# Performance work log

Hardware: AMD Instinct MI355X
Metric: run time of the kernel (lower is better)

The kernel has to match this reference:

```python
import jax, jax.numpy as jnp
import numpy as np
from jax import lax

T, B, DIM, N = 1024, 64, 512, 64


def setup_inputs() -> dict:
    key = jax.random.key(0)
    k1, k2 = jax.random.split(key)
    x = jax.random.normal(k1, (T, B, DIM), dtype=jnp.float32)
    # xavier-uniform-like scale for fused projection [4n, dim]
    lim = float(np.sqrt(6.0 / (N + DIM)))
    W_kvqm = jax.random.uniform(k2, (4 * N, DIM), dtype=jnp.float32, minval=-lim, maxval=lim)
    return {
        "x": x,
        "S0": jnp.zeros((B, N, N), dtype=jnp.float32),
        "M0": jnp.zeros((B, N, N), dtype=jnp.float32),
        "W_kvqm": W_kvqm,
        "B_S": jnp.full((N, N), 2.0, dtype=jnp.float32),
        "B_M": jnp.full((N, N), 2.5, dtype=jnp.float32),
    }


def reference(x, S0, M0, W_kvqm, B_S, B_M):
    n = S0.shape[1]
    # fused projection for all timesteps: [T, B, 4n]
    proj = jnp.einsum('tbd,nd->tbn', x, W_kvqm)
    k_all, v_all, q_all, m_all = jnp.split(proj, 4, axis=-1)

    def step(carry, inp):
        S, M = carry
        k, v, q, m_vec = inp
        k_norm = k / (jnp.linalg.norm(k, axis=-1, keepdims=True) + 1e-6)
        m_norm = m_vec / (jnp.linalg.norm(m_vec, axis=-1, keepdims=True) + 1e-6)
        # S update gated by M
        M_k = jnp.einsum('bij,bj->bi', M, k_norm)
        G_S = jax.nn.sigmoid(M + jnp.einsum('bi,bj->bij', M_k, k_norm) + B_S)
        s_delta = v - jnp.einsum('bij,bj->bi', S, k_norm)
        S = G_S * S + jnp.einsum('bi,bj->bij', s_delta, k_norm)
        # M update gated by (new) S
        S_m = jnp.einsum('bij,bj->bi', S, m_norm)
        G_M = jax.nn.sigmoid(S + jnp.einsum('bi,bj->bij', S_m, m_norm) + B_M)
        m_delta = s_delta - jnp.einsum('bij,bj->bi', M, m_norm)
        M = G_M * M + jnp.einsum('bi,bj->bij', m_delta, m_norm)
        Sq = jnp.einsum('bij,bj->bi', S, q)
        out = Sq * jax.nn.silu(Sq)
        return (S, M), out

    (S, M), output = lax.scan(step, (S0, M0), (k_all, v_all, q_all, m_all))
    return output, S, M
```

## Files before the change

### kernel.cpp

```cpp
#include <hip/hip_runtime.h>
#include <cstddef>

#define T_STEPS 1024
#define BATCH   64
#define DIMK    512
#define NDIM    64
#define PROJW   256
#define STEPSTRIDE (BATCH * PROJW)

__device__ __forceinline__ float sigmoidf_(float x) {
    return __builtin_amdgcn_rcpf(1.0f + __expf(-x));
}

template<int CTRL>
__device__ __forceinline__ float dpp_mov(float x) {
    return __int_as_float(__builtin_amdgcn_update_dpp(
        0, __float_as_int(x), CTRL, 0xF, 0xF, true));
}
__device__ __forceinline__ float redrow32(float x) {
    x += dpp_mov<0x128>(x);
    x += dpp_mov<0x124>(x);
    x += dpp_mov<0x122>(x);
    x += dpp_mov<0x121>(x);
    x += __shfl_xor(x, 16);
    return x;
}

__global__ __launch_bounds__(256) void proj_gemm(const float* __restrict__ X,
                                                 const float* __restrict__ W,
                                                 float* __restrict__ C) {
    __shared__ float As[16][132];
    __shared__ float Bs[16][132];
    const int tid  = threadIdx.x;
    const int row0 = blockIdx.x * 128;
    const int col0 = blockIdx.y * 128;
    const int tx4  = (tid & 15) << 2;
    const int ty4  = (tid >> 4) << 2;
    const int lm   = tid >> 2;
    const int lk   = (tid & 3) << 2;

    const float* Arow0 = X + (size_t)(row0 + lm)      * DIMK + lk;
    const float* Arow1 = X + (size_t)(row0 + lm + 64) * DIMK + lk;
    const float* Brow0 = W + (size_t)(col0 + lm)      * DIMK + lk;
    const float* Brow1 = W + (size_t)(col0 + lm + 64) * DIMK + lk;

    float acc[8][8] = {};
    float4 pa0, pa1, pb0, pb1;

    pa0 = *(const float4*)(Arow0);
    pa1 = *(const float4*)(Arow1);
    pb0 = *(const float4*)(Brow0);
    pb1 = *(const float4*)(Brow1);

    for (int tile = 0; tile < DIMK / 16; ++tile) {
        __syncthreads();
        As[lk+0][lm]    = pa0.x; As[lk+1][lm]    = pa0.y; As[lk+2][lm]    = pa0.z; As[lk+3][lm]    = pa0.w;
        As[lk+0][lm+64] = pa1.x; As[lk+1][lm+64] = pa1.y; As[lk+2][lm+64] = pa1.z; As[lk+3][lm+64] = pa1.w;
        Bs[lk+0][lm]    = pb0.x; Bs[lk+1][lm]    = pb0.y; Bs[lk+2][lm]    = pb0.z; Bs[lk+3][lm]    = pb0.w;
        Bs[lk+0][lm+64] = pb1.x; Bs[lk+1][lm+64] = pb1.y; Bs[lk+2][lm+64] = pb1.z; Bs[lk+3][lm+64] = pb1.w;
        __syncthreads();
        if (tile + 1 < DIMK / 16) {
            const int kb = (tile + 1) * 16;
            pa0 = *(const float4*)(Arow0 + kb);
            pa1 = *(const float4*)(Arow1 + kb);
            pb0 = *(const float4*)(Brow0 + kb);
            pb1 = *(const float4*)(Brow1 + kb);
        }
        #pragma unroll 8
        for (int k = 0; k < 16; ++k) {
            const float4 a0v = *(const float4*)&As[k][ty4];
            const float4 a1v = *(const float4*)&As[k][64 + ty4];
            const float4 b0v = *(const float4*)&Bs[k][tx4];
            const float4 b1v = *(const float4*)&Bs[k][64 + tx4];
            const float a[8]  = {a0v.x, a0v.y, a0v.z, a0v.w, a1v.x, a1v.y, a1v.z, a1v.w};
            const float bb[8] = {b0v.x, b0v.y, b0v.z, b0v.w, b1v.x, b1v.y, b1v.z, b1v.w};
            #pragma unroll
            for (int i2 = 0; i2 < 8; ++i2)
                #pragma unroll
                for (int j2 = 0; j2 < 8; ++j2)
                    acc[i2][j2] = fmaf(a[i2], bb[j2], acc[i2][j2]);
        }
    }

    #pragma unroll
    for (int h = 0; h < 2; ++h) {
        #pragma unroll
        for (int r = 0; r < 4; ++r) {
            const size_t R = (size_t)(row0 + h * 64 + ty4 + r) * PROJW + col0;
            float4 o0 = {acc[h*4+r][0], acc[h*4+r][1], acc[h*4+r][2], acc[h*4+r][3]};
            float4 o1 = {acc[h*4+r][4], acc[h*4+r][5], acc[h*4+r][6], acc[h*4+r][7]};
            *(float4*)&C[R + tx4]      = o0;
            *(float4*)&C[R + 64 + tx4] = o1;
        }
    }
}

__global__ __launch_bounds__(256) void normalize_km(float* __restrict__ proj) {
    const int p    = blockIdx.x * 4 + (threadIdx.x >> 6);
    const int lane = threadIdx.x & 63;
    float* base = proj + (size_t)p * PROJW;
    const float k = base[lane];
    const float m = base[192 + lane];
    float sk = k * k, sm = m * m;
    #pragma unroll
    for (int d = 1; d < 64; d <<= 1) {
        sk += __shfl_xor(sk, d);
        sm += __shfl_xor(sm, d);
    }
    base[lane]       = k / (sqrtf(sk) + 1e-6f);
    base[192 + lane] = m / (sqrtf(sm) + 1e-6f);
}

__global__ __launch_bounds__(256) void recur_kernel(const float* __restrict__ proj,
                                                    const float* __restrict__ S0,
                                                    const float* __restrict__ M0,
                                                    const float* __restrict__ BSmat,
                                                    const float* __restrict__ BMmat,
                                                    float* __restrict__ outp,
                                                    float* __restrict__ Sout,
                                                    float* __restrict__ Mout) {
    const int tid = threadIdx.x;
    const int b   = blockIdx.x & 63;
    const int oct = blockIdx.x >> 6;
    const int lr  = tid >> 5;
    const int i   = (oct << 3) + lr;
    const int l32 = tid & 31;
    const int j0  = l32 << 1;

    float S[2], Mr[2], BSr[2], BMr[2];
    const size_t smoff = ((size_t)b * NDIM + i) * NDIM + j0;
    { float2 t2 = *(const float2*)&S0[smoff];                    S[0]=t2.x;  S[1]=t2.y;  }
    { float2 t2 = *(const float2*)&M0[smoff];                    Mr[0]=t2.x; Mr[1]=t2.y; }
    { float2 t2 = *(const float2*)&BSmat[(size_t)i * NDIM + j0]; BSr[0]=t2.x;BSr[1]=t2.y;}
    { float2 t2 = *(const float2*)&BMmat[(size_t)i * NDIM + j0]; BMr[0]=t2.x;BMr[1]=t2.y;}

    const float* pb = proj + (size_t)b * PROJW;

    auto step = [&](int t, float2 kn2, float2 q2, float2 mn2, float v_i) {
        float Mk = Mr[0] * kn2.x; Mk = fmaf(Mr[1], kn2.y, Mk);
        float Sk = S[0]  * kn2.x; Sk = fmaf(S[1],  kn2.y, Sk);
        float Mm = Mr[0] * mn2.x; Mm = fmaf(Mr[1], mn2.y, Mm);
        Mk = redrow32(Mk); Sk = redrow32(Sk); Mm = redrow32(Mm);
        const float sd = v_i - Sk;

        {
            const float g0 = sigmoidf_(fmaf(Mk, kn2.x, Mr[0]) + BSr[0]);
            const float g1 = sigmoidf_(fmaf(Mk, kn2.y, Mr[1]) + BSr[1]);
            S[0] = fmaf(g0, S[0], sd * kn2.x);
            S[1] = fmaf(g1, S[1], sd * kn2.y);
        }
        float Sm = S[0] * mn2.x; Sm = fmaf(S[1], mn2.y, Sm);
        float Sq = S[0] * q2.x;  Sq = fmaf(S[1], q2.y,  Sq);
        Sm = redrow32(Sm); Sq = redrow32(Sq);
        const float md = sd - Mm;

        {
            const float g0 = sigmoidf_(fmaf(Sm, mn2.x, S[0]) + BMr[0]);
            const float g1 = sigmoidf_(fmaf(Sm, mn2.y, S[1]) + BMr[1]);
            Mr[0] = fmaf(g0, Mr[0], md * mn2.x);
            Mr[1] = fmaf(g1, Mr[1], md * mn2.y);
        }
        if (l32 == 0) {
            outp[(size_t)t * (BATCH * NDIM) + b * NDIM + i] = Sq * Sq * sigmoidf_(Sq);
        }
    };

#define DECL_SET(s) float2 kn##s, q##s, mn##s; float vi##s;
#define LOAD_SET(s, tt) { \
        const int t_ = ((tt) < T_STEPS) ? (tt) : (T_STEPS - 1); \
        const float* r_ = pb + (size_t)t_ * STEPSTRIDE; \
        kn##s = *(const float2*)(r_ + j0); \
        q##s  = *(const float2*)(r_ + 128 + j0); \
        mn##s = *(const float2*)(r_ + 192 + j0); \
        vi##s = r_[64 + i]; }

    DECL_SET(0) DECL_SET(1) DECL_SET(2) DECL_SET(3)
    LOAD_SET(0, 0) LOAD_SET(1, 1) LOAD_SET(2, 2) LOAD_SET(3, 3)

    for (int t = 0; t < T_STEPS; t += 4) {
        step(t + 0, kn0, q0, mn0, vi0); LOAD_SET(0, t + 4);
        step(t + 1, kn1, q1, mn1, vi1); LOAD_SET(1, t + 5);
        step(t + 2, kn2, q2, mn2, vi2); LOAD_SET(2, t + 6);
        step(t + 3, kn3, q3, mn3, vi3); LOAD_SET(3, t + 7);
    }
#undef DECL_SET
#undef LOAD_SET

    { float2 o = {S[0], S[1]};   *(float2*)&Sout[smoff] = o; }
    { float2 o = {Mr[0], Mr[1]}; *(float2*)&Mout[smoff] = o; }
}

extern "C" void kernel_launch(void* const* d_in, const int* in_sizes, int n_in,
                              void* d_out, int out_size, void* d_ws, size_t ws_size,
                              hipStream_t stream) {
    const float* x   = (const float*)d_in[0];
    const float* S0  = (const float*)d_in[1];
    const float* M0  = (const float*)d_in[2];
    const float* W   = (const float*)d_in[3];
    const float* BS  = (const float*)d_in[4];
    const float* BMb = (const float*)d_in[5];
    float* out = (float*)d_out;

    float* proj = (float*)d_ws;

    dim3 g1(512, 2), b1(256);
    proj_gemm<<<g1, b1, 0, stream>>>(x, W, proj);

    normalize_km<<<dim3(T_STEPS * BATCH / 4), dim3(256), 0, stream>>>(proj);

    float* Sout = out + (size_t)T_STEPS * BATCH * NDIM;
    float* Mout = Sout + (size_t)BATCH * NDIM * NDIM;
    recur_kernel<<<dim3(BATCH * 8), dim3(256), 0, stream>>>(proj, S0, M0, BS, BMb,
                                                            out, Sout, Mout);
}
```

Before: 734.5 us.

## Use split-bf16 MFMA GEMM for projection and permlane16_swap in row reduction

Splits x and W into bf16 high and low parts, then computes the projection with bf16 MFMA instructions using three passes (hi*hi, hi*lo, lo*hi). This aims to replace the FP32 FMA GEMM with matrix-core throughput while keeping close to FP32 accuracy. The row reduction in the recurrence swaps a shuffle for permlane16_swap, and the final loop iteration is peeled so the load index no longer needs clamping. The change adds two conversion kernels and needs extra workspace; if the workspace is too small it falls back to the old GEMM.

After: 741.9 us. Within noise of the previous version (+1.0%).

```diff
diff --git a/kernel.cpp b/kernel.cpp
--- a/kernel.cpp
+++ b/kernel.cpp
@@ -8,6 +8,10 @@
 #define PROJW   256
 #define STEPSTRIDE (BATCH * PROJW)
 
+typedef __attribute__((ext_vector_type(8))) short short8;
+typedef __attribute__((ext_vector_type(4))) float f32x4;
+typedef __attribute__((ext_vector_type(2))) unsigned int uint2v;
+
 __device__ __forceinline__ float sigmoidf_(float x) {
     return __builtin_amdgcn_rcpf(1.0f + __expf(-x));
 }
@@ -22,8 +26,99 @@
     x += dpp_mov<0x124>(x);
     x += dpp_mov<0x122>(x);
     x += dpp_mov<0x121>(x);
-    x += __shfl_xor(x, 16);
-    return x;
+    uint2v r = __builtin_amdgcn_permlane16_swap(__float_as_uint(x), __float_as_uint(x),
+                                                false, false);
+    return __uint_as_float(r.x) + __uint_as_float(r.y);
+}
+
+__device__ __forceinline__ unsigned short f2bf(float f) {
+    unsigned u = __float_as_uint(f);
+    return (unsigned short)((u + 0x7FFFu + ((u >> 16) & 1u)) >> 16);
+}
+
+__global__ __launch_bounds__(256) void cvt_split(const float* __restrict__ src,
+                                                 unsigned short* __restrict__ hi,
+                                                 unsigned short* __restrict__ lo,
+                                                 int n4) {
+    for (int idx = blockIdx.x * 256 + threadIdx.x; idx < n4; idx += gridDim.x * 256) {
+        float4 v = ((const float4*)src)[idx];
+        ushort4 h, l;
+#define CV(c, fld) { unsigned short hb = f2bf(v.c); h.fld = hb; \
+                     float hf = __uint_as_float(((unsigned)hb) << 16); \
+                     l.fld = f2bf(v.c - hf); }
+        CV(x, x) CV(y, y) CV(z, z) CV(w, w)
+#undef CV
+        ((ushort4*)hi)[idx] = h;
+        ((ushort4*)lo)[idx] = l;
+    }
+}
+
+__global__ __launch_bounds__(256) void proj_gemm_mfma(
+        const unsigned short* __restrict__ Xhi, const unsigned short* __restrict__ Xlo,
+        const unsigned short* __restrict__ Whi, const unsigned short* __restrict__ Wlo,
+        float* __restrict__ C) {
+    __shared__ unsigned short sA[128][40];
+    __shared__ unsigned short sB[128][40];
+    const int tid  = threadIdx.x;
+    const int row0 = blockIdx.x * 128;
+    const int col0 = blockIdx.y * 128;
+    const int w    = tid >> 6;
+    const int l    = tid & 63;
+    const int wr   = w >> 1, wc = w & 1;
+    const int l15  = l & 15, lh = l >> 4;
+    const int r0   = tid >> 2;
+    const int p0   = (tid & 3) << 3;
+
+    f32x4 acc[4][4] = {};
+    uint4 ra0, ra1, rb0, rb1;
+
+    ra0 = *(const uint4*)(Xhi + (size_t)(row0 + r0)      * DIMK + p0);
+    ra1 = *(const uint4*)(Xhi + (size_t)(row0 + 64 + r0) * DIMK + p0);
+    rb0 = *(const uint4*)(Whi + (size_t)(col0 + r0)      * DIMK + p0);
+    rb1 = *(const uint4*)(Whi + (size_t)(col0 + 64 + r0) * DIMK + p0);
+
+    for (int it = 0; it < 48; ++it) {
+        __syncthreads();
+        *(uint4*)&sA[r0][p0]      = ra0;
+        *(uint4*)&sA[64 + r0][p0] = ra1;
+        *(uint4*)&sB[r0][p0]      = rb0;
+        *(uint4*)&sB[64 + r0][p0] = rb1;
+        __syncthreads();
+        if (it + 1 < 48) {
+            const int s   = (it + 1) >> 4;
+            const int kin = ((it + 1) & 15) << 5;
+            const unsigned short* Ap = (s == 2) ? Xlo : Xhi;
+            const unsigned short* Bp = (s == 1) ? Wlo : Whi;
+            ra0 = *(const uint4*)(Ap + (size_t)(row0 + r0)      * DIMK + kin + p0);
+            ra1 = *(const uint4*)(Ap + (size_t)(row0 + 64 + r0) * DIMK + kin + p0);
+            rb0 = *(const uint4*)(Bp + (size_t)(col0 + r0)      * DIMK + kin + p0);
+            rb1 = *(const uint4*)(Bp + (size_t)(col0 + 64 + r0) * DIMK + kin + p0);
+        }
+        short8 af[4], bf_[4];
+        #pragma unroll
+        for (int mi = 0; mi < 4; ++mi)
+            af[mi] = *(const short8*)&sA[wr * 64 + mi * 16 + l15][lh * 8];
+        #pragma unroll
+        for (int ni = 0; ni < 4; ++ni)
+            bf_[ni] = *(const short8*)&sB[wc * 64 + ni * 16 + l15][lh * 8];
+        #pragma unroll
+        for (int mi = 0; mi < 4; ++mi)
+            #pragma unroll
+            for (int ni = 0; ni < 4; ++ni)
+                acc[mi][ni] = __builtin_amdgcn_mfma_f32_16x16x32_bf16(
+                    af[mi], bf_[ni], acc[mi][ni], 0, 0, 0);
+    }
+
+    #pragma unroll
+    for (int mi = 0; mi < 4; ++mi)
+        #pragma unroll
+        for (int ni = 0; ni < 4; ++ni)
+            #pragma unroll
+            for (int r = 0; r < 4; ++r) {
+                const int row = row0 + wr * 64 + mi * 16 + lh * 4 + r;
+                const int col = col0 + wc * 64 + ni * 16 + l15;
+                C[(size_t)row * PROJW + col] = acc[mi][ni][r];
+            }
 }
 
 __global__ __launch_bounds__(256) void proj_gemm(const float* __restrict__ X,
@@ -45,12 +140,10 @@
     const float* Brow1 = W + (size_t)(col0 + lm + 64) * DIMK + lk;
 
     float acc[8][8] = {};
-    float4 pa0, pa1, pb0, pb1;
-
-    pa0 = *(const float4*)(Arow0);
-    pa1 = *(const float4*)(Arow1);
-    pb0 = *(const float4*)(Brow0);
-    pb1 = *(const float4*)(Brow1);
+    float4 pa0 = *(const float4*)(Arow0);
+    float4 pa1 = *(const float4*)(Arow1);
+    float4 pb0 = *(const float4*)(Brow0);
+    float4 pb1 = *(const float4*)(Brow1);
 
     for (int tile = 0; tile < DIMK / 16; ++tile) {
         __syncthreads();
@@ -81,9 +174,8 @@
                     acc[i2][j2] = fmaf(a[i2], bb[j2], acc[i2][j2]);
         }
     }
-
     #pragma unroll
-    for (int h = 0; h < 2; ++h) {
+    for (int h = 0; h < 2; ++h)
         #pragma unroll
         for (int r = 0; r < 4; ++r) {
             const size_t R = (size_t)(row0 + h * 64 + ty4 + r) * PROJW + col0;
@@ -92,7 +184,6 @@
             *(float4*)&C[R + tx4]      = o0;
             *(float4*)&C[R + 64 + tx4] = o1;
         }
-    }
 }
 
 __global__ __launch_bounds__(256) void normalize_km(float* __restrict__ proj) {
@@ -142,7 +233,6 @@
         float Mm = Mr[0] * mn2.x; Mm = fmaf(Mr[1], mn2.y, Mm);
         Mk = redrow32(Mk); Sk = redrow32(Sk); Mm = redrow32(Mm);
         const float sd = v_i - Sk;
-
         {
             const float g0 = sigmoidf_(fmaf(Mk, kn2.x, Mr[0]) + BSr[0]);
             const float g1 = sigmoidf_(fmaf(Mk, kn2.y, Mr[1]) + BSr[1]);
@@ -153,7 +243,6 @@
         float Sq = S[0] * q2.x;  Sq = fmaf(S[1], q2.y,  Sq);
         Sm = redrow32(Sm); Sq = redrow32(Sq);
         const float md = sd - Mm;
-
         {
             const float g0 = sigmoidf_(fmaf(Sm, mn2.x, S[0]) + BMr[0]);
             const float g1 = sigmoidf_(fmaf(Sm, mn2.y, S[1]) + BMr[1]);
@@ -167,8 +256,7 @@
 
 #define DECL_SET(s) float2 kn##s, q##s, mn##s; float vi##s;
 #define LOAD_SET(s, tt) { \
-        const int t_ = ((tt) < T_STEPS) ? (tt) : (T_STEPS - 1); \
-        const float* r_ = pb + (size_t)t_ * STEPSTRIDE; \
+        const float* r_ = pb + (size_t)(tt) * STEPSTRIDE; \
         kn##s = *(const float2*)(r_ + j0); \
         q##s  = *(const float2*)(r_ + 128 + j0); \
         mn##s = *(const float2*)(r_ + 192 + j0); \
@@ -177,12 +265,16 @@
     DECL_SET(0) DECL_SET(1) DECL_SET(2) DECL_SET(3)
     LOAD_SET(0, 0) LOAD_SET(1, 1) LOAD_SET(2, 2) LOAD_SET(3, 3)
 
-    for (int t = 0; t < T_STEPS; t += 4) {
+    for (int t = 0; t < T_STEPS - 4; t += 4) {
         step(t + 0, kn0, q0, mn0, vi0); LOAD_SET(0, t + 4);
         step(t + 1, kn1, q1, mn1, vi1); LOAD_SET(1, t + 5);
         step(t + 2, kn2, q2, mn2, vi2); LOAD_SET(2, t + 6);
         step(t + 3, kn3, q3, mn3, vi3); LOAD_SET(3, t + 7);
     }
+    step(T_STEPS - 4, kn0, q0, mn0, vi0);
+    step(T_STEPS - 3, kn1, q1, mn1, vi1);
+    step(T_STEPS - 2, kn2, q2, mn2, vi2);
+    step(T_STEPS - 1, kn3, q3, mn3, vi3);
 #undef DECL_SET
 #undef LOAD_SET
 
@@ -201,10 +293,24 @@
     const float* BMb = (const float*)d_in[5];
     float* out = (float*)d_out;
 
+    const size_t XN = (size_t)T_STEPS * BATCH * DIMK;
+    const size_t WN = (size_t)PROJW * DIMK;
+    const size_t PROJB = (size_t)T_STEPS * BATCH * PROJW * sizeof(float);
+    const size_t need  = PROJB + 2 * XN * 2 + 2 * WN * 2;
+
     float* proj = (float*)d_ws;
 
-    dim3 g1(512, 2), b1(256);
-    proj_gemm<<<g1, b1, 0, stream>>>(x, W, proj);
+    if (ws_size >= need) {
+        unsigned short* Xhi = (unsigned short*)((char*)d_ws + PROJB);
+        unsigned short* Xlo = Xhi + XN;
+        unsigned short* Whi = Xlo + XN;
+        unsigned short* Wlo = Whi + WN;
+        cvt_split<<<dim3(2048), dim3(256), 0, stream>>>(x, Xhi, Xlo, (int)(XN / 4));
+        cvt_split<<<dim3(128),  dim3(256), 0, stream>>>(W, Whi, Wlo, (int)(WN / 4));
+        proj_gemm_mfma<<<dim3(512, 2), dim3(256), 0, stream>>>(Xhi, Xlo, Whi, Wlo, proj);
+    } else {
+        proj_gemm<<<dim3(512, 2), dim3(256), 0, stream>>>(x, W, proj);
+    }
 
     normalize_km<<<dim3(T_STEPS * BATCH / 4), dim3(256), 0, stream>>>(proj);
 
```
